# Performance work log

Hardware: AMD Instinct MI355X
Metric: run time of the kernel (lower is better)

Reference implementation:

```python
import jax, jax.numpy as jnp
import numpy as np

ALIGN_SCALE = 3.0
UNIF_SCALE = 1.0
EPS = 1e-12  # torch F.normalize eps


def _normalize(x):
    n = jnp.linalg.norm(x, axis=-1, keepdims=True)
    return x / jnp.maximum(n, EPS)


def _unif_loss(a, b):
    # log(mean(exp(-2 * ||a_i - b_j||^2))) over all N*M pairs, fused via GEMM identity
    sq_a = jnp.sum(a * a, axis=1)  # [N]
    sq_b = jnp.sum(b * b, axis=1)  # [M]
    # squared distances: ||a||^2 + ||b||^2 - 2 a.b, clipped at 0 for numerics
    d2 = jnp.maximum(sq_a[:, None] + sq_b[None, :] - 2.0 * (a @ b.T), 0.0)  # [N, M]
    return jnp.log(jnp.mean(jnp.exp(-2.0 * d2)))


def setup_inputs() -> dict:
    key = jax.random.key(0)
    k1, k2 = jax.random.split(key)
    N, D = 8192, 512
    return {
        "image_embed": jax.random.normal(k1, (N, D), dtype=jnp.float32),
        "text_embed": jax.random.normal(k2, (N, D), dtype=jnp.float32),
    }


def reference(image_embed, text_embed):
    img = _normalize(image_embed)
    txt = _normalize(text_embed)
    # alignment: mean squared L2 between paired embeddings
    diff = img - txt
    align_loss = jnp.mean(jnp.sum(diff * diff, axis=1))
    # single device: gathered-all tensors equal the local tensors
    text_unif = _unif_loss(txt, txt)
    image_unif = _unif_loss(img, img)
    unif_loss = (text_unif + image_unif) / 2.0
    return ALIGN_SCALE * align_loss + UNIF_SCALE * unif_loss
```

## Files before the change

kernel.cpp:

```cpp
#include <hip/hip_runtime.h>
#include <hip/hip_bf16.h>


#define NROWS 8192
#define DBYTES 512
#define NT    64
#define NTILES 2080
#define SCALE_SPLAT 0x75757575

typedef __attribute__((ext_vector_type(8)))  int   int8v;
typedef __attribute__((ext_vector_type(4)))  int   int4v;
typedef __attribute__((ext_vector_type(16))) float float16v;

__device__ inline void load_lds16(const void* g, void* l) {
    __builtin_amdgcn_global_load_lds(
        (const __attribute__((address_space(1))) void*)g,
        (__attribute__((address_space(3))) void*)l, 16, 0, 0);
}

__device__ inline int swz(int r) { return (r ^ (r >> 3)) & 7; }

__global__ __launch_bounds__(256) void normalize_kernel(
    const float* __restrict__ img, const float* __restrict__ txt,
    unsigned char* __restrict__ nimg, unsigned char* __restrict__ ntxt,
    float* __restrict__ alignp,
    float* __restrict__ S)
{
    if (blockIdx.x == 0 && threadIdx.x < 64) S[threadIdx.x] = 0.0f;

    const int lane = threadIdx.x & 63;
    const int wave = threadIdx.x >> 6;
    const int row  = blockIdx.x * 4 + wave;

    const float4* pi = (const float4*)(img + (size_t)row * 512);
    const float4* pt = (const float4*)(txt + (size_t)row * 512);
    const float4 i0 = pi[lane], i1 = pi[lane + 64];
    const float4 t0 = pt[lane], t1 = pt[lane + 64];

    float ssi = i0.x*i0.x + i0.y*i0.y + i0.z*i0.z + i0.w*i0.w
              + i1.x*i1.x + i1.y*i1.y + i1.z*i1.z + i1.w*i1.w;
    float sst = t0.x*t0.x + t0.y*t0.y + t0.z*t0.z + t0.w*t0.w
              + t1.x*t1.x + t1.y*t1.y + t1.z*t1.z + t1.w*t1.w;
    float dot = i0.x*t0.x + i0.y*t0.y + i0.z*t0.z + i0.w*t0.w
              + i1.x*t1.x + i1.y*t1.y + i1.z*t1.z + i1.w*t1.w;

    #pragma unroll
    for (int off = 1; off < 64; off <<= 1) {
        ssi += __shfl_xor(ssi, off);
        sst += __shfl_xor(sst, off);
        dot += __shfl_xor(dot, off);
    }
    const float inv_i = 1.0f / fmaxf(sqrtf(ssi), 1e-12f);
    const float inv_t = 1.0f / fmaxf(sqrtf(sst), 1e-12f);
    const float si = 1024.0f * inv_i;
    const float st = 1024.0f * inv_t;

    int p0 = __builtin_amdgcn_cvt_pk_fp8_f32(i0.x*si, i0.y*si, 0, false);
    p0     = __builtin_amdgcn_cvt_pk_fp8_f32(i0.z*si, i0.w*si, p0, true);
    int p1 = __builtin_amdgcn_cvt_pk_fp8_f32(i1.x*si, i1.y*si, 0, false);
    p1     = __builtin_amdgcn_cvt_pk_fp8_f32(i1.z*si, i1.w*si, p1, true);
    int q0 = __builtin_amdgcn_cvt_pk_fp8_f32(t0.x*st, t0.y*st, 0, false);
    q0     = __builtin_amdgcn_cvt_pk_fp8_f32(t0.z*st, t0.w*st, q0, true);
    int q1 = __builtin_amdgcn_cvt_pk_fp8_f32(t1.x*st, t1.y*st, 0, false);
    q1     = __builtin_amdgcn_cvt_pk_fp8_f32(t1.z*st, t1.w*st, q1, true);

    int* oi = (int*)(nimg + (size_t)row * DBYTES);
    int* ot = (int*)(ntxt + (size_t)row * DBYTES);
    oi[lane] = p0; oi[lane + 64] = p1;
    ot[lane] = q0; ot[lane + 64] = q1;

    __shared__ float r4[4];
    if (lane == 0) r4[wave] = dot * inv_i * inv_t;
    __syncthreads();
    if (threadIdx.x == 0)
        alignp[blockIdx.x] = r4[0] + r4[1] + r4[2] + r4[3];
}

__global__ __launch_bounds__(256) void gram_kernel(
    const unsigned char* __restrict__ A0,
    const unsigned char* __restrict__ A1,
    float* __restrict__ S)
{
    const int t = blockIdx.x;
    int i = (int)((129.0f - sqrtf(129.0f * 129.0f - 8.0f * (float)t)) * 0.5f);
    while ((i + 1) * (129 - (i + 1)) / 2 <= t) ++i;
    while (i * (129 - i) / 2 > t) --i;
    const int j = i + (t - i * (129 - i) / 2);

    const unsigned char* __restrict__ A = blockIdx.y ? A1 : A0;
    const int tid  = threadIdx.x;
    const int lane = tid & 63;
    const int wave = tid >> 6;
    const int wm = wave & 1, wn = wave >> 1;
    const int lr = lane & 31;
    const int h  = lane >> 5;

    const unsigned char* gA = A + (size_t)i * 128 * DBYTES;
    const unsigned char* gB = A + (size_t)j * 128 * DBYTES;

    __shared__ __align__(16) unsigned char ldsA[128 * 128];
    __shared__ __align__(16) unsigned char ldsB[128 * 128];

    float16v acc[2][2];
    #pragma unroll
    for (int a = 0; a < 2; ++a)
        #pragma unroll
        for (int b = 0; b < 2; ++b)
            #pragma unroll
            for (int r = 0; r < 16; ++r) acc[a][b][r] = 0.0f;

    for (int k0 = 0; k0 < DBYTES; k0 += 128) {
        #pragma unroll
        for (int rnd = 0; rnd < 4; ++rnd) {
            const int slot = rnd * 4096 + tid * 16;
            const int r    = slot >> 7;
            const int cp   = (slot >> 4) & 7;
            const int cl   = cp ^ swz(r);
            load_lds16(gA + (size_t)r * DBYTES + k0 + cl * 16, &ldsA[slot]);
            load_lds16(gB + (size_t)r * DBYTES + k0 + cl * 16, &ldsB[slot]);
        }
        __syncthreads();

        #pragma unroll
        for (int kk = 0; kk < 2; ++kk) {
            const int cbase = kk * 4 + h * 2;
            int8v av[2], bv[2];
            #pragma unroll
            for (int mt = 0; mt < 2; ++mt) {
                const int r = wm * 64 + mt * 32 + lr;
                const int s = swz(r);
                const int4v q0 = *(const int4v*)&ldsA[r * 128 + ((cbase    ) ^ s) * 16];
                const int4v q1 = *(const int4v*)&ldsA[r * 128 + ((cbase + 1) ^ s) * 16];
                av[mt][0]=q0[0]; av[mt][1]=q0[1]; av[mt][2]=q0[2]; av[mt][3]=q0[3];
                av[mt][4]=q1[0]; av[mt][5]=q1[1]; av[mt][6]=q1[2]; av[mt][7]=q1[3];
            }
            #pragma unroll
            for (int nt = 0; nt < 2; ++nt) {
                const int r = wn * 64 + nt * 32 + lr;
                const int s = swz(r);
                const int4v q0 = *(const int4v*)&ldsB[r * 128 + ((cbase    ) ^ s) * 16];
                const int4v q1 = *(const int4v*)&ldsB[r * 128 + ((cbase + 1) ^ s) * 16];
                bv[nt][0]=q0[0]; bv[nt][1]=q0[1]; bv[nt][2]=q0[2]; bv[nt][3]=q0[3];
                bv[nt][4]=q1[0]; bv[nt][5]=q1[1]; bv[nt][6]=q1[2]; bv[nt][7]=q1[3];
            }
            #pragma unroll
            for (int mt = 0; mt < 2; ++mt)
                #pragma unroll
                for (int nt = 0; nt < 2; ++nt)
                    acc[mt][nt] = __builtin_amdgcn_mfma_scale_f32_32x32x64_f8f6f4(
                        av[mt], bv[nt], acc[mt][nt],
                        0, 0,
                        0, SCALE_SPLAT,
                        0, SCALE_SPLAT);
        }
        __syncthreads();
    }

    float s = 0.0f;
    #pragma unroll
    for (int mt = 0; mt < 2; ++mt)
        #pragma unroll
        for (int nt = 0; nt < 2; ++nt)
            #pragma unroll
            for (int r2 = 0; r2 < 16; ++r2) {
                const float g = acc[mt][nt][r2];
                s += __expf(4.0f * fminf(g, 1.0f) - 4.0f);
            }
    #pragma unroll
    for (int off = 32; off; off >>= 1) s += __shfl_down(s, off);
    __shared__ float ps[4];
    if (lane == 0) ps[wave] = s;
    __syncthreads();
    if (tid == 0) {
        const float tot = ps[0] + ps[1] + ps[2] + ps[3];
        const float w = (i == j) ? 1.0f : 2.0f;
        atomicAdd(&S[blockIdx.y * 32 + (blockIdx.x & 31)], tot * w);
    }
}

__global__ __launch_bounds__(256) void finalize_kernel(
    const float* __restrict__ S,
    const float* __restrict__ alignp,
    float* __restrict__ out)
{
    const int tid = threadIdx.x;
    float a = 0.0f;
    #pragma unroll
    for (int k = 0; k < 8; ++k) a += alignp[tid + 256 * k];
    #pragma unroll
    for (int off = 32; off; off >>= 1) a += __shfl_down(a, off);
    __shared__ float r4[4];
    if ((tid & 63) == 0) r4[tid >> 6] = a;
    __syncthreads();
    if (tid == 0) {
        const double A = (double)r4[0] + r4[1] + r4[2] + r4[3];
        double si = 0.0, st = 0.0;
        for (int k = 0; k < 32; ++k) { si += S[k]; st += S[32 + k]; }
        const double align = 2.0 - 2.0 * A / (double)NROWS;
        const double n2 = (double)NROWS * (double)NROWS;
        const double unif = 0.5 * (log(si / n2) + log(st / n2));
        out[0] = (float)(3.0 * align + unif);
    }
}

extern "C" void kernel_launch(void* const* d_in, const int* in_sizes, int n_in,
                              void* d_out, int out_size, void* d_ws, size_t ws_size,
                              hipStream_t stream) {
    const float* img = (const float*)d_in[0];
    const float* txt = (const float*)d_in[1];
    char* ws = (char*)d_ws;
    unsigned char* nimg = (unsigned char*)ws;
    unsigned char* ntxt = (unsigned char*)(ws + (size_t)NROWS * DBYTES);
    float* S      = (float*)(ws + 2 * (size_t)NROWS * DBYTES);
    float* alignp = S + 64;

    normalize_kernel<<<NROWS / 4, 256, 0, stream>>>(img, txt, nimg, ntxt, alignp, S);
    dim3 grid(NTILES, 2);
    gram_kernel<<<grid, 256, 0, stream>>>(nimg, ntxt, S);
    finalize_kernel<<<1, 256, 0, stream>>>(S, alignp, (float*)d_out);
}
```

Before: 127.9 us.

## Load MFMA operands directly from global memory, dropping LDS staging

The gram kernel no longer stages the 128x128 fp8 tiles in shared memory with swizzled global-to-LDS loads and barriers. Each lane now reads its MFMA operand fragments straight from global memory, with the K loop fully unrolled so all loads can be issued early. This removes the LDS round trip and the __syncthreads calls. In exchange, operand data is no longer shared between waves, so each row is fetched twice from global memory or cache, and the per-lane 32-byte strided reads may coalesce less well. Register pressure also rises.

New measurement: 198.8 us. 1.55x slower.

```diff
diff --git a/kernel.cpp b/kernel.cpp
--- a/kernel.cpp
+++ b/kernel.cpp
@@ -11,14 +11,6 @@
 typedef __attribute__((ext_vector_type(8)))  int   int8v;
 typedef __attribute__((ext_vector_type(4)))  int   int4v;
 typedef __attribute__((ext_vector_type(16))) float float16v;
-
-__device__ inline void load_lds16(const void* g, void* l) {
-    __builtin_amdgcn_global_load_lds(
-        (const __attribute__((address_space(1))) void*)g,
-        (__attribute__((address_space(3))) void*)l, 16, 0, 0);
-}
-
-__device__ inline int swz(int r) { return (r ^ (r >> 3)) & 7; }
 
 __global__ __launch_bounds__(256) void normalize_kernel(
     const float* __restrict__ img, const float* __restrict__ txt,
@@ -95,11 +87,10 @@
     const int lr = lane & 31;
     const int h  = lane >> 5;
 
-    const unsigned char* gA = A + (size_t)i * 128 * DBYTES;
-    const unsigned char* gB = A + (size_t)j * 128 * DBYTES;
-
-    __shared__ __align__(16) unsigned char ldsA[128 * 128];
-    __shared__ __align__(16) unsigned char ldsB[128 * 128];
+    const unsigned char* pa0 = A + ((size_t)(i * 128 + wm * 64      + lr)) * DBYTES + h * 32;
+    const unsigned char* pa1 = pa0 + 32 * DBYTES;
+    const unsigned char* pb0 = A + ((size_t)(j * 128 + wn * 64      + lr)) * DBYTES + h * 32;
+    const unsigned char* pb1 = pb0 + 32 * DBYTES;
 
     float16v acc[2][2];
     #pragma unroll
@@ -109,51 +100,36 @@
             #pragma unroll
             for (int r = 0; r < 16; ++r) acc[a][b][r] = 0.0f;
 
-    for (int k0 = 0; k0 < DBYTES; k0 += 128) {
+    #pragma unroll
+    for (int k0 = 0; k0 < DBYTES; k0 += 64) {
+        int8v av[2], bv[2];
+        {
+            const int4v a00 = *(const int4v*)(pa0 + k0);
+            const int4v a01 = *(const int4v*)(pa0 + k0 + 16);
+            const int4v a10 = *(const int4v*)(pa1 + k0);
+            const int4v a11 = *(const int4v*)(pa1 + k0 + 16);
+            const int4v b00 = *(const int4v*)(pb0 + k0);
+            const int4v b01 = *(const int4v*)(pb0 + k0 + 16);
+            const int4v b10 = *(const int4v*)(pb1 + k0);
+            const int4v b11 = *(const int4v*)(pb1 + k0 + 16);
+            av[0][0]=a00[0]; av[0][1]=a00[1]; av[0][2]=a00[2]; av[0][3]=a00[3];
+            av[0][4]=a01[0]; av[0][5]=a01[1]; av[0][6]=a01[2]; av[0][7]=a01[3];
+            av[1][0]=a10[0]; av[1][1]=a10[1]; av[1][2]=a10[2]; av[1][3]=a10[3];
+            av[1][4]=a11[0]; av[1][5]=a11[1]; av[1][6]=a11[2]; av[1][7]=a11[3];
+            bv[0][0]=b00[0]; bv[0][1]=b00[1]; bv[0][2]=b00[2]; bv[0][3]=b00[3];
+            bv[0][4]=b01[0]; bv[0][5]=b01[1]; bv[0][6]=b01[2]; bv[0][7]=b01[3];
+            bv[1][0]=b10[0]; bv[1][1]=b10[1]; bv[1][2]=b10[2]; bv[1][3]=b10[3];
+            bv[1][4]=b11[0]; bv[1][5]=b11[1]; bv[1][6]=b11[2]; bv[1][7]=b11[3];
+        }
         #pragma unroll
-        for (int rnd = 0; rnd < 4; ++rnd) {
-            const int slot = rnd * 4096 + tid * 16;
-            const int r    = slot >> 7;
-            const int cp   = (slot >> 4) & 7;
-            const int cl   = cp ^ swz(r);
-            load_lds16(gA + (size_t)r * DBYTES + k0 + cl * 16, &ldsA[slot]);
-            load_lds16(gB + (size_t)r * DBYTES + k0 + cl * 16, &ldsB[slot]);
-        }
-        __syncthreads();
-
-        #pragma unroll
-        for (int kk = 0; kk < 2; ++kk) {
-            const int cbase = kk * 4 + h * 2;
-            int8v av[2], bv[2];
+        for (int mt = 0; mt < 2; ++mt)
             #pragma unroll
-            for (int mt = 0; mt < 2; ++mt) {
-                const int r = wm * 64 + mt * 32 + lr;
-                const int s = swz(r);
-                const int4v q0 = *(const int4v*)&ldsA[r * 128 + ((cbase    ) ^ s) * 16];
-                const int4v q1 = *(const int4v*)&ldsA[r * 128 + ((cbase + 1) ^ s) * 16];
-                av[mt][0]=q0[0]; av[mt][1]=q0[1]; av[mt][2]=q0[2]; av[mt][3]=q0[3];
-                av[mt][4]=q1[0]; av[mt][5]=q1[1]; av[mt][6]=q1[2]; av[mt][7]=q1[3];
-            }
-            #pragma unroll
-            for (int nt = 0; nt < 2; ++nt) {
-                const int r = wn * 64 + nt * 32 + lr;
-                const int s = swz(r);
-                const int4v q0 = *(const int4v*)&ldsB[r * 128 + ((cbase    ) ^ s) * 16];
-                const int4v q1 = *(const int4v*)&ldsB[r * 128 + ((cbase + 1) ^ s) * 16];
-                bv[nt][0]=q0[0]; bv[nt][1]=q0[1]; bv[nt][2]=q0[2]; bv[nt][3]=q0[3];
-                bv[nt][4]=q1[0]; bv[nt][5]=q1[1]; bv[nt][6]=q1[2]; bv[nt][7]=q1[3];
-            }
-            #pragma unroll
-            for (int mt = 0; mt < 2; ++mt)
-                #pragma unroll
-                for (int nt = 0; nt < 2; ++nt)
-                    acc[mt][nt] = __builtin_amdgcn_mfma_scale_f32_32x32x64_f8f6f4(
-                        av[mt], bv[nt], acc[mt][nt],
-                        0, 0,
-                        0, SCALE_SPLAT,
-                        0, SCALE_SPLAT);
-        }
-        __syncthreads();
+            for (int nt = 0; nt < 2; ++nt)
+                acc[mt][nt] = __builtin_amdgcn_mfma_scale_f32_32x32x64_f8f6f4(
+                    av[mt], bv[nt], acc[mt][nt],
+                    0, 0,
+                    0, SCALE_SPLAT,
+                    0, SCALE_SPLAT);
     }
 
     float s = 0.0f;
```

## Process four Gram tiles per block, keeping the A row-tile in registers

Applied to the files above, without the earlier changes.

Each gram block now walks four consecutive upper-triangular tiles. The A row-panel (128x512 fp8) is loaded once into registers and reused, and only the B panel is reloaded per tile. The full K=512 panel is staged in one 64KB LDS buffer, replacing the four 128-wide k-steps, and the block count drops by a factor of four. The aim is to cut redundant A loads, loop syncs and per-tile launch cost, at the price of much higher register pressure (launch bounds of 256 threads, 2 blocks per CU), serialized load-then-compute with no double buffering, and fewer blocks for load balancing.

New measurement: 246.5 us. 1.93x slower.

```diff
diff --git a/kernel.cpp b/kernel.cpp
--- a/kernel.cpp
+++ b/kernel.cpp
@@ -6,6 +6,8 @@
 #define DBYTES 512
 #define NT    64
 #define NTILES 2080
+#define JTILES 4
+#define NBLK (NTILES / JTILES)
 #define SCALE_SPLAT 0x75757575
 
 typedef __attribute__((ext_vector_type(8)))  int   int8v;
@@ -19,6 +21,7 @@
 }
 
 __device__ inline int swz(int r) { return (r ^ (r >> 3)) & 7; }
+__device__ inline int chsw(int c, int r) { return (c & ~7) | ((c & 7) ^ swz(r)); }
 
 __global__ __launch_bounds__(256) void normalize_kernel(
     const float* __restrict__ img, const float* __restrict__ txt,
@@ -76,17 +79,11 @@
         alignp[blockIdx.x] = r4[0] + r4[1] + r4[2] + r4[3];
 }
 
-__global__ __launch_bounds__(256) void gram_kernel(
+__global__ __launch_bounds__(256, 2) void gram_kernel(
     const unsigned char* __restrict__ A0,
     const unsigned char* __restrict__ A1,
     float* __restrict__ S)
 {
-    const int t = blockIdx.x;
-    int i = (int)((129.0f - sqrtf(129.0f * 129.0f - 8.0f * (float)t)) * 0.5f);
-    while ((i + 1) * (129 - (i + 1)) / 2 <= t) ++i;
-    while (i * (129 - i) / 2 > t) --i;
-    const int j = i + (t - i * (129 - i) / 2);
-
     const unsigned char* __restrict__ A = blockIdx.y ? A1 : A0;
     const int tid  = threadIdx.x;
     const int lane = tid & 63;
@@ -95,51 +92,80 @@
     const int lr = lane & 31;
     const int h  = lane >> 5;
 
-    const unsigned char* gA = A + (size_t)i * 128 * DBYTES;
-    const unsigned char* gB = A + (size_t)j * 128 * DBYTES;
-
-    __shared__ __align__(16) unsigned char ldsA[128 * 128];
-    __shared__ __align__(16) unsigned char ldsB[128 * 128];
-
-    float16v acc[2][2];
-    #pragma unroll
-    for (int a = 0; a < 2; ++a)
-        #pragma unroll
-        for (int b = 0; b < 2; ++b)
-            #pragma unroll
-            for (int r = 0; r < 16; ++r) acc[a][b][r] = 0.0f;
-
-    for (int k0 = 0; k0 < DBYTES; k0 += 128) {
-        #pragma unroll
-        for (int rnd = 0; rnd < 4; ++rnd) {
-            const int slot = rnd * 4096 + tid * 16;
-            const int r    = slot >> 7;
-            const int cp   = (slot >> 4) & 7;
-            const int cl   = cp ^ swz(r);
-            load_lds16(gA + (size_t)r * DBYTES + k0 + cl * 16, &ldsA[slot]);
-            load_lds16(gB + (size_t)r * DBYTES + k0 + cl * 16, &ldsB[slot]);
+    const int t0i = blockIdx.x * JTILES;
+    int i = (int)((129.0f - sqrtf(129.0f * 129.0f - 8.0f * (float)t0i)) * 0.5f);
+    while ((i + 1) * (129 - (i + 1)) / 2 <= t0i) ++i;
+    while (i * (129 - i) / 2 > t0i) --i;
+    int j = i + (t0i - i * (129 - i) / 2);
+
+    __shared__ __align__(16) unsigned char lds[128 * 512];
+    __shared__ float ps[4];
+
+    const int sr_off = tid >> 5;
+    const int scp    = tid & 31;
+
+    int8v av[2][8];
+    int cur_i = -1;
+    float s = 0.0f;
+
+    for (int tt = 0; tt < JTILES; ++tt) {
+        __syncthreads();
+
+        if (i != cur_i) {
+            const unsigned char* gA = A + (size_t)i * 128 * DBYTES;
+            #pragma unroll
+            for (int rnd = 0; rnd < 16; ++rnd) {
+                const int r  = rnd * 8 + sr_off;
+                const int cl = chsw(scp, r);
+                load_lds16(gA + (size_t)r * DBYTES + cl * 16,
+                           &lds[r * DBYTES + scp * 16]);
+            }
+            __syncthreads();
+            #pragma unroll
+            for (int mt = 0; mt < 2; ++mt) {
+                const int r = wm * 64 + mt * 32 + lr;
+                #pragma unroll
+                for (int ks = 0; ks < 8; ++ks) {
+                    const int c = ks * 4 + h * 2;
+                    const int4v q0 = *(const int4v*)&lds[r * DBYTES + chsw(c,     r) * 16];
+                    const int4v q1 = *(const int4v*)&lds[r * DBYTES + chsw(c + 1, r) * 16];
+                    av[mt][ks][0]=q0[0]; av[mt][ks][1]=q0[1];
+                    av[mt][ks][2]=q0[2]; av[mt][ks][3]=q0[3];
+                    av[mt][ks][4]=q1[0]; av[mt][ks][5]=q1[1];
+                    av[mt][ks][6]=q1[2]; av[mt][ks][7]=q1[3];
+                }
+            }
+            cur_i = i;
+            __syncthreads();
+        }
+
+        const unsigned char* gB = A + (size_t)j * 128 * DBYTES;
+        #pragma unroll
+        for (int rnd = 0; rnd < 16; ++rnd) {
+            const int r  = rnd * 8 + sr_off;
+            const int cl = chsw(scp, r);
+            load_lds16(gB + (size_t)r * DBYTES + cl * 16,
+                       &lds[r * DBYTES + scp * 16]);
         }
         __syncthreads();
 
-        #pragma unroll
-        for (int kk = 0; kk < 2; ++kk) {
-            const int cbase = kk * 4 + h * 2;
-            int8v av[2], bv[2];
-            #pragma unroll
-            for (int mt = 0; mt < 2; ++mt) {
-                const int r = wm * 64 + mt * 32 + lr;
-                const int s = swz(r);
-                const int4v q0 = *(const int4v*)&ldsA[r * 128 + ((cbase    ) ^ s) * 16];
-                const int4v q1 = *(const int4v*)&ldsA[r * 128 + ((cbase + 1) ^ s) * 16];
-                av[mt][0]=q0[0]; av[mt][1]=q0[1]; av[mt][2]=q0[2]; av[mt][3]=q0[3];
-                av[mt][4]=q1[0]; av[mt][5]=q1[1]; av[mt][6]=q1[2]; av[mt][7]=q1[3];
-            }
+        float16v acc[2][2];
+        #pragma unroll
+        for (int a = 0; a < 2; ++a)
+            #pragma unroll
+            for (int b = 0; b < 2; ++b)
+                #pragma unroll
+                for (int r = 0; r < 16; ++r) acc[a][b][r] = 0.0f;
+
+        #pragma unroll
+        for (int ks = 0; ks < 8; ++ks) {
+            const int c = ks * 4 + h * 2;
+            int8v bv[2];
             #pragma unroll
             for (int nt = 0; nt < 2; ++nt) {
                 const int r = wn * 64 + nt * 32 + lr;
-                const int s = swz(r);
-                const int4v q0 = *(const int4v*)&ldsB[r * 128 + ((cbase    ) ^ s) * 16];
-                const int4v q1 = *(const int4v*)&ldsB[r * 128 + ((cbase + 1) ^ s) * 16];
+                const int4v q0 = *(const int4v*)&lds[r * DBYTES + chsw(c,     r) * 16];
+                const int4v q1 = *(const int4v*)&lds[r * DBYTES + chsw(c + 1, r) * 16];
                 bv[nt][0]=q0[0]; bv[nt][1]=q0[1]; bv[nt][2]=q0[2]; bv[nt][3]=q0[3];
                 bv[nt][4]=q1[0]; bv[nt][5]=q1[1]; bv[nt][6]=q1[2]; bv[nt][7]=q1[3];
             }
@@ -148,33 +174,34 @@
                 #pragma unroll
                 for (int nt = 0; nt < 2; ++nt)
                     acc[mt][nt] = __builtin_amdgcn_mfma_scale_f32_32x32x64_f8f6f4(
-                        av[mt], bv[nt], acc[mt][nt],
+                        av[mt][ks], bv[nt], acc[mt][nt],
                         0, 0,
                         0, SCALE_SPLAT,
                         0, SCALE_SPLAT);
         }
-        __syncthreads();
-    }
-
-    float s = 0.0f;
-    #pragma unroll
-    for (int mt = 0; mt < 2; ++mt)
-        #pragma unroll
-        for (int nt = 0; nt < 2; ++nt)
-            #pragma unroll
-            for (int r2 = 0; r2 < 16; ++r2) {
-                const float g = acc[mt][nt][r2];
-                s += __expf(4.0f * fminf(g, 1.0f) - 4.0f);
-            }
+
+        const float w = (i == j) ? 1.0f : 2.0f;
+        #pragma unroll
+        for (int mt = 0; mt < 2; ++mt)
+            #pragma unroll
+            for (int nt = 0; nt < 2; ++nt)
+                #pragma unroll
+                for (int r2 = 0; r2 < 16; ++r2) {
+                    const float g = acc[mt][nt][r2];
+                    s += w * __expf(4.0f * fminf(g, 1.0f) - 4.0f);
+                }
+
+        ++j;
+        if (j == NT) { ++i; j = i; }
+    }
+
     #pragma unroll
     for (int off = 32; off; off >>= 1) s += __shfl_down(s, off);
-    __shared__ float ps[4];
     if (lane == 0) ps[wave] = s;
     __syncthreads();
     if (tid == 0) {
         const float tot = ps[0] + ps[1] + ps[2] + ps[3];
-        const float w = (i == j) ? 1.0f : 2.0f;
-        atomicAdd(&S[blockIdx.y * 32 + (blockIdx.x & 31)], tot * w);
+        atomicAdd(&S[blockIdx.y * 32 + (blockIdx.x & 31)], tot);
     }
 }
 
@@ -215,7 +242,7 @@
     float* alignp = S + 64;
 
     normalize_kernel<<<NROWS / 4, 256, 0, stream>>>(img, txt, nimg, ntxt, alignp, S);
-    dim3 grid(NTILES, 2);
+    dim3 grid(NBLK, 2);
     gram_kernel<<<grid, 256, 0, stream>>>(nimg, ntxt, S);
     finalize_kernel<<<1, 256, 0, stream>>>(S, alignp, (float*)d_out);
 }
```

## Enlarge gram tile to 256x128 with per-wave triangular weighting

Applied to the files above, without the earlier changes.

Changes the Gram-matrix tiling from 128x128 upper-triangular tiles to 256x128 tiles, so each block loads a 256-row A panel and reuses it across twice as many MFMAs, cutting global/LDS traffic per flop. The triangular mapping is reworked so the grid has 1056 blocks. Each wave's contribution is weighted 0/1/2 according to whether its 128-row half lies below, on, or above the diagonal. This computes some redundant lower-triangle tiles that are then discarded. It also doubles accumulator registers and LDS usage, with launch bounds requesting 2 blocks per CU.

New measurement: 123.9 us. -3.1%, faster.

```diff
diff --git a/kernel.cpp b/kernel.cpp
--- a/kernel.cpp
+++ b/kernel.cpp
@@ -5,7 +5,7 @@
 #define NROWS 8192
 #define DBYTES 512
 #define NT    64
-#define NTILES 2080
+#define NBLK  1056
 #define SCALE_SPLAT 0x75757575
 
 typedef __attribute__((ext_vector_type(8)))  int   int8v;
@@ -76,16 +76,16 @@
         alignp[blockIdx.x] = r4[0] + r4[1] + r4[2] + r4[3];
 }
 
-__global__ __launch_bounds__(256) void gram_kernel(
+__global__ __launch_bounds__(256, 2) void gram_kernel(
     const unsigned char* __restrict__ A0,
     const unsigned char* __restrict__ A1,
     float* __restrict__ S)
 {
-    const int t = blockIdx.x;
-    int i = (int)((129.0f - sqrtf(129.0f * 129.0f - 8.0f * (float)t)) * 0.5f);
-    while ((i + 1) * (129 - (i + 1)) / 2 <= t) ++i;
-    while (i * (129 - i) / 2 > t) --i;
-    const int j = i + (t - i * (129 - i) / 2);
+    const int b = blockIdx.x;
+    int I = (int)((65.0f - sqrtf(4225.0f - 4.0f * (float)b)) * 0.5f);
+    while ((I + 1) * (64 - I) <= b) ++I;
+    while (I * (65 - I) > b) --I;
+    const int j = 2 * I + (b - I * (65 - I));
 
     const unsigned char* __restrict__ A = blockIdx.y ? A1 : A0;
     const int tid  = threadIdx.x;
@@ -95,56 +95,59 @@
     const int lr = lane & 31;
     const int h  = lane >> 5;
 
-    const unsigned char* gA = A + (size_t)i * 128 * DBYTES;
+    const unsigned char* gA = A + (size_t)I * 256 * DBYTES;
     const unsigned char* gB = A + (size_t)j * 128 * DBYTES;
 
-    __shared__ __align__(16) unsigned char ldsA[128 * 128];
+    __shared__ __align__(16) unsigned char ldsA[256 * 128];
     __shared__ __align__(16) unsigned char ldsB[128 * 128];
 
-    float16v acc[2][2];
-    #pragma unroll
-    for (int a = 0; a < 2; ++a)
-        #pragma unroll
-        for (int b = 0; b < 2; ++b)
-            #pragma unroll
-            for (int r = 0; r < 16; ++r) acc[a][b][r] = 0.0f;
+    float16v acc[4][2];
+    #pragma unroll
+    for (int a = 0; a < 4; ++a)
+        #pragma unroll
+        for (int c = 0; c < 2; ++c)
+            #pragma unroll
+            for (int r = 0; r < 16; ++r) acc[a][c][r] = 0.0f;
 
     for (int k0 = 0; k0 < DBYTES; k0 += 128) {
+        #pragma unroll
+        for (int rnd = 0; rnd < 8; ++rnd) {
+            const int slot = rnd * 4096 + tid * 16;
+            const int r    = slot >> 7;
+            const int cp   = (slot >> 4) & 7;
+            const int cl   = cp ^ swz(r);
+            load_lds16(gA + (size_t)r * DBYTES + k0 + cl * 16, &ldsA[slot]);
+        }
         #pragma unroll
         for (int rnd = 0; rnd < 4; ++rnd) {
             const int slot = rnd * 4096 + tid * 16;
             const int r    = slot >> 7;
             const int cp   = (slot >> 4) & 7;
             const int cl   = cp ^ swz(r);
-            load_lds16(gA + (size_t)r * DBYTES + k0 + cl * 16, &ldsA[slot]);
             load_lds16(gB + (size_t)r * DBYTES + k0 + cl * 16, &ldsB[slot]);
         }
         __syncthreads();
 
         #pragma unroll
         for (int kk = 0; kk < 2; ++kk) {
-            const int cbase = kk * 4 + h * 2;
-            int8v av[2], bv[2];
-            #pragma unroll
-            for (int mt = 0; mt < 2; ++mt) {
-                const int r = wm * 64 + mt * 32 + lr;
-                const int s = swz(r);
-                const int4v q0 = *(const int4v*)&ldsA[r * 128 + ((cbase    ) ^ s) * 16];
-                const int4v q1 = *(const int4v*)&ldsA[r * 128 + ((cbase + 1) ^ s) * 16];
-                av[mt][0]=q0[0]; av[mt][1]=q0[1]; av[mt][2]=q0[2]; av[mt][3]=q0[3];
-                av[mt][4]=q1[0]; av[mt][5]=q1[1]; av[mt][6]=q1[2]; av[mt][7]=q1[3];
+            const int c0 = kk * 4 + h * 2;
+            int8v av[4], bv[2];
+            #pragma unroll
+            for (int mt = 0; mt < 4; ++mt) {
+                const int r = wm * 128 + mt * 32 + lr;
+                const int s0 = swz(r);
+                *((int4v*)&av[mt])     = *(const int4v*)&ldsA[r * 128 + ((c0    ) ^ s0) * 16];
+                *((int4v*)&av[mt] + 1) = *(const int4v*)&ldsA[r * 128 + ((c0 + 1) ^ s0) * 16];
             }
             #pragma unroll
             for (int nt = 0; nt < 2; ++nt) {
                 const int r = wn * 64 + nt * 32 + lr;
-                const int s = swz(r);
-                const int4v q0 = *(const int4v*)&ldsB[r * 128 + ((cbase    ) ^ s) * 16];
-                const int4v q1 = *(const int4v*)&ldsB[r * 128 + ((cbase + 1) ^ s) * 16];
-                bv[nt][0]=q0[0]; bv[nt][1]=q0[1]; bv[nt][2]=q0[2]; bv[nt][3]=q0[3];
-                bv[nt][4]=q1[0]; bv[nt][5]=q1[1]; bv[nt][6]=q1[2]; bv[nt][7]=q1[3];
+                const int s0 = swz(r);
+                *((int4v*)&bv[nt])     = *(const int4v*)&ldsB[r * 128 + ((c0    ) ^ s0) * 16];
+                *((int4v*)&bv[nt] + 1) = *(const int4v*)&ldsB[r * 128 + ((c0 + 1) ^ s0) * 16];
             }
             #pragma unroll
-            for (int mt = 0; mt < 2; ++mt)
+            for (int mt = 0; mt < 4; ++mt)
                 #pragma unroll
                 for (int nt = 0; nt < 2; ++nt)
                     acc[mt][nt] = __builtin_amdgcn_mfma_scale_f32_32x32x64_f8f6f4(
@@ -156,9 +159,11 @@
         __syncthreads();
     }
 
+    const int r128 = 2 * I + wm;
+    const float wv = (j > r128) ? 2.0f : ((j == r128) ? 1.0f : 0.0f);
     float s = 0.0f;
     #pragma unroll
-    for (int mt = 0; mt < 2; ++mt)
+    for (int mt = 0; mt < 4; ++mt)
         #pragma unroll
         for (int nt = 0; nt < 2; ++nt)
             #pragma unroll
@@ -166,6 +171,7 @@
                 const float g = acc[mt][nt][r2];
                 s += __expf(4.0f * fminf(g, 1.0f) - 4.0f);
             }
+    s *= wv;
     #pragma unroll
     for (int off = 32; off; off >>= 1) s += __shfl_down(s, off);
     __shared__ float ps[4];
@@ -173,8 +179,7 @@
     __syncthreads();
     if (tid == 0) {
         const float tot = ps[0] + ps[1] + ps[2] + ps[3];
-        const float w = (i == j) ? 1.0f : 2.0f;
-        atomicAdd(&S[blockIdx.y * 32 + (blockIdx.x & 31)], tot * w);
+        atomicAdd(&S[blockIdx.y * 32 + (blockIdx.x & 31)], tot);
     }
 }
 
@@ -215,7 +220,7 @@
     float* alignp = S + 64;
 
     normalize_kernel<<<NROWS / 4, 256, 0, stream>>>(img, txt, nimg, ntxt, alignp, S);
-    dim3 grid(NTILES, 2);
+    dim3 grid(NBLK, 2);
     gram_kernel<<<grid, 256, 0, stream>>>(nimg, ntxt, S);
     finalize_kernel<<<1, 256, 0, stream>>>(S, alignp, (float*)d_out);
 }
```
